# Optimization experiments

Measured on AMD Instinct MI355X. Metric: run time of the kernel, lower is better.

## Reference

```python
import jax, jax.numpy as jnp
import numpy as np

PI = float(np.pi)


def _mat(rows):
    # rows: 4 lists of 4 [..., ] arrays -> [..., 4, 4]
    return jnp.stack([jnp.stack(r, axis=-1) for r in rows], axis=-2)


def _local_frames(q):
    """q: [..., 7] joint angles -> list of 8 local [..., 4, 4] transforms."""
    z = jnp.zeros_like(q[..., 0])
    o = jnp.ones_like(z)

    def cs(a):
        return jnp.cos(a), jnp.sin(a)

    c0, s0 = cs(q[..., 0])
    c1, s1 = cs(q[..., 1])
    c2, s2 = cs(q[..., 2] - 0.5 * PI)
    c3, s3 = cs(q[..., 3])
    c4, s4 = cs(q[..., 4])
    c5, s5 = cs(q[..., 5] + 0.5 * PI)
    c6, s6 = cs(q[..., 6] - 0.5 * PI)

    m0 = _mat([[c0, -s0, z, z], [s0, c0, z, z], [z, z, o, z], [z, z, z, o]])
    m1 = _mat([[c1, -s1, z, z], [z, z, -o, z], [s1, c1, z, z], [z, z, z, o]])
    m2 = _mat([[c2, -s2, z, z], [z, z, o, 0.4 * o], [-s2, -c2, z, z], [z, z, z, o]])
    m3 = _mat([[c3, -s3, z, z], [z, z, -o, z], [s3, c3, z, z], [z, z, z, o]])
    m4 = _mat([[-c4, s4, z, z], [z, z, o, 0.39 * o], [s4, c4, z, z], [z, z, z, o]])
    m5 = _mat([[c5, -s5, z, z], [z, z, -o, z], [s5, c5, z, z], [z, z, z, o]])
    m6 = _mat([[c6, -s6, z, z], [z, z, -o, z], [s6, c6, z, z], [z, z, z, o]])
    m7 = _mat([[-o, z, z, z], [z, z, o, 0.118 * o], [z, o, z, z], [z, z, z, o]])
    return [m0, m1, m2, m3, m4, m5, m6, m7]


def setup_inputs() -> dict:
    key = jax.random.key(0)
    x = jax.random.normal(key, (2000000, 7), dtype=jnp.float32)
    return {"x": x}


def reference(x):
    mats = _local_frames(x)
    frames = [mats[0]]
    f = mats[0]
    for m in mats[1:]:  # fixed chain of 7 tiny 4x4 matmuls over batch
        f = jnp.einsum("...ij,...jk->...ik", f, m)
        frames.append(f)
    return jnp.stack(frames, axis=-3)  # [..., 8, 4, 4]
```

## Files before the change

kernel.cpp:

```cpp
#include <hip/hip_runtime.h>

namespace {

struct V3 { float x, y, z; };

__device__ inline V3 v3(float x, float y, float z) { return {x, y, z}; }
__device__ inline V3 vadd(V3 a, V3 b) { return {a.x + b.x, a.y + b.y, a.z + b.z}; }
__device__ inline V3 vsub(V3 a, V3 b) { return {a.x - b.x, a.y - b.y, a.z - b.z}; }
__device__ inline V3 vmul(float s, V3 a) { return {s * a.x, s * a.y, s * a.z}; }
__device__ inline V3 vneg(V3 a) { return {-a.x, -a.y, -a.z}; }

__device__ inline void stage_frame(float4* p, V3 c0, V3 c1, V3 c2, V3 c3) {
    p[0] = make_float4(c0.x, c1.x, c2.x, c3.x);
    p[1] = make_float4(c0.y, c1.y, c2.y, c3.y);
    p[2] = make_float4(c0.z, c1.z, c2.z, c3.z);
    p[3] = make_float4(0.f, 0.f, 0.f, 1.f);
}

}

#define LPAD 9

__global__ __launch_bounds__(256) void fk_chain_kernel(const float* __restrict__ q,
                                                       float4* __restrict__ out,
                                                       int n)
{
    __shared__ float4 lds[4 * 64 * LPAD];

    const int tid  = threadIdx.x;
    const int lane = tid & 63;
    const int wave = tid >> 6;
    const long long e0 = (long long)blockIdx.x * 256 + (long long)wave * 64;
    if (e0 >= n) return;
    const long long i = e0 + lane;
    const bool active = i < (long long)n;

    const float* qi = q + (active ? i : 0) * 7;
    const float HPI = 1.57079632679489662f;

    float qv[7];
    #pragma unroll
    for (int k = 0; k < 7; ++k) qv[k] = qi[k];

    float c[7], s[7];
    __sincosf(qv[0], &s[0], &c[0]);
    __sincosf(qv[1], &s[1], &c[1]);
    __sincosf(qv[2] - HPI, &s[2], &c[2]);
    __sincosf(qv[3], &s[3], &c[3]);
    __sincosf(qv[4], &s[4], &c[4]);
    __sincosf(qv[5] + HPI, &s[5], &c[5]);
    __sincosf(qv[6] - HPI, &s[6], &c[6]);

    float4* ldsW = lds + wave * (64 * LPAD);
    float4* myS  = ldsW + lane * LPAD;

    const int rk = lane & 7;
    const int re = lane >> 3;
    float4* gb = out + e0 * 32 + (long long)re * 32 + rk;

    V3 f0 = v3(c[0], s[0], 0.f);
    V3 f1 = v3(-s[0], c[0], 0.f);
    V3 f2 = v3(0.f, 0.f, 1.f);
    V3 f3 = v3(0.f, 0.f, 0.f);

    #define TYPE_A(cc, ss)                                 \
        {                                                  \
            V3 t0 = vadd(vmul((cc), f0), vmul((ss), f2));  \
            V3 t1 = vsub(vmul((cc), f2), vmul((ss), f0));  \
            V3 t2 = vneg(f1);                              \
            f0 = t0; f1 = t1; f2 = t2;                     \
        }

    #define FLUSH(p)                                                      \
        {                                                                 \
            _Pragma("unroll")                                             \
            for (int j = 0; j < 8; ++j) {                                 \
                int e = j * 8 + re;                                       \
                float4 v = ldsW[e * LPAD + rk];                           \
                if (e0 + e < (long long)n) gb[(long long)j * 256 + (p) * 8] = v; \
            }                                                             \
        }

    stage_frame(myS + 0, f0, f1, f2, f3);
    TYPE_A(c[1], s[1]);
    stage_frame(myS + 4, f0, f1, f2, f3);
    FLUSH(0);

    {
        V3 t0 = vsub(vmul(c[2], f0), vmul(s[2], f2));
        V3 t1 = vneg(vadd(vmul(s[2], f0), vmul(c[2], f2)));
        V3 t2 = f1;
        f3 = vadd(vmul(0.4f, f1), f3);
        f0 = t0; f1 = t1; f2 = t2;
    }
    stage_frame(myS + 0, f0, f1, f2, f3);
    TYPE_A(c[3], s[3]);
    stage_frame(myS + 4, f0, f1, f2, f3);
    FLUSH(1);

    {
        V3 t0 = vsub(vmul(s[4], f2), vmul(c[4], f0));
        V3 t1 = vadd(vmul(s[4], f0), vmul(c[4], f2));
        V3 t2 = f1;
        f3 = vadd(vmul(0.39f, f1), f3);
        f0 = t0; f1 = t1; f2 = t2;
    }
    stage_frame(myS + 0, f0, f1, f2, f3);
    TYPE_A(c[5], s[5]);
    stage_frame(myS + 4, f0, f1, f2, f3);
    FLUSH(2);

    TYPE_A(c[6], s[6]);
    stage_frame(myS + 0, f0, f1, f2, f3);
    {
        V3 t0 = vneg(f0);
        V3 t1 = f2;
        V3 t2 = f1;
        f3 = vadd(vmul(0.118f, f1), f3);
        f0 = t0; f1 = t1; f2 = t2;
    }
    stage_frame(myS + 4, f0, f1, f2, f3);
    FLUSH(3);

    #undef TYPE_A
    #undef FLUSH
}

extern "C" void kernel_launch(void* const* d_in, const int* in_sizes, int n_in,
                              void* d_out, int out_size, void* d_ws, size_t ws_size,
                              hipStream_t stream) {
    const float* x = (const float*)d_in[0];
    float* out = (float*)d_out;
    int n = in_sizes[0] / 7;
    int block = 256;
    int grid = (n + block - 1) / block;
    fk_chain_kernel<<<grid, block, 0, stream>>>(x, (float4*)out, n);
}
```

Before: 211.6 us.

## Stage all eight frames in LDS then write one coalesced contiguous block

Each element's 8 frames are staged in LDS at a padded stride. After one barrier the 64-thread block writes its 32 KB output region contiguously, replacing the four interleaved partial flushes. Blocks shrink to a single wave and out-of-range lanes read a valid input row. The write is already bandwidth-bound, so the cleaner write pattern may help only a little, while the larger per-block LDS and the barrier could reduce overlap.

```diff
diff --git a/kernel.cpp b/kernel.cpp
--- a/kernel.cpp
+++ b/kernel.cpp
@@ -19,23 +19,20 @@
 
 }
 
-#define LPAD 9
+#define LSTRIDE 33
 
-__global__ __launch_bounds__(256) void fk_chain_kernel(const float* __restrict__ q,
-                                                       float4* __restrict__ out,
-                                                       int n)
+__global__ __launch_bounds__(64) void fk_chain_kernel(const float* __restrict__ q,
+                                                      float4* __restrict__ out,
+                                                      int n)
 {
-    __shared__ float4 lds[4 * 64 * LPAD];
+    __shared__ float4 lds[64 * LSTRIDE];
 
-    const int tid  = threadIdx.x;
-    const int lane = tid & 63;
-    const int wave = tid >> 6;
-    const long long e0 = (long long)blockIdx.x * 256 + (long long)wave * 64;
-    if (e0 >= n) return;
+    const int lane = threadIdx.x;
+    const long long e0 = (long long)blockIdx.x * 64;
     const long long i = e0 + lane;
     const bool active = i < (long long)n;
 
-    const float* qi = q + (active ? i : 0) * 7;
+    const float* qi = q + (active ? i : (long long)(n - 1)) * 7;
     const float HPI = 1.57079632679489662f;
 
     float qv[7];
@@ -51,12 +48,7 @@
     __sincosf(qv[5] + HPI, &s[5], &c[5]);
     __sincosf(qv[6] - HPI, &s[6], &c[6]);
 
-    float4* ldsW = lds + wave * (64 * LPAD);
-    float4* myS  = ldsW + lane * LPAD;
-
-    const int rk = lane & 7;
-    const int re = lane >> 3;
-    float4* gb = out + e0 * 32 + (long long)re * 32 + rk;
+    float4* myS = lds + lane * LSTRIDE;
 
     V3 f0 = v3(c[0], s[0], 0.f);
     V3 f1 = v3(-s[0], c[0], 0.f);
@@ -71,20 +63,10 @@
             f0 = t0; f1 = t1; f2 = t2;                     \
         }
 
-    #define FLUSH(p)                                                      \
-        {                                                                 \
-            _Pragma("unroll")                                             \
-            for (int j = 0; j < 8; ++j) {                                 \
-                int e = j * 8 + re;                                       \
-                float4 v = ldsW[e * LPAD + rk];                           \
-                if (e0 + e < (long long)n) gb[(long long)j * 256 + (p) * 8] = v; \
-            }                                                             \
-        }
+    stage_frame(myS + 0, f0, f1, f2, f3);
 
-    stage_frame(myS + 0, f0, f1, f2, f3);
     TYPE_A(c[1], s[1]);
     stage_frame(myS + 4, f0, f1, f2, f3);
-    FLUSH(0);
 
     {
         V3 t0 = vsub(vmul(c[2], f0), vmul(s[2], f2));
@@ -93,10 +75,10 @@
         f3 = vadd(vmul(0.4f, f1), f3);
         f0 = t0; f1 = t1; f2 = t2;
     }
-    stage_frame(myS + 0, f0, f1, f2, f3);
+    stage_frame(myS + 8, f0, f1, f2, f3);
+
     TYPE_A(c[3], s[3]);
-    stage_frame(myS + 4, f0, f1, f2, f3);
-    FLUSH(1);
+    stage_frame(myS + 12, f0, f1, f2, f3);
 
     {
         V3 t0 = vsub(vmul(s[4], f2), vmul(c[4], f0));
@@ -105,13 +87,14 @@
         f3 = vadd(vmul(0.39f, f1), f3);
         f0 = t0; f1 = t1; f2 = t2;
     }
-    stage_frame(myS + 0, f0, f1, f2, f3);
+    stage_frame(myS + 16, f0, f1, f2, f3);
+
     TYPE_A(c[5], s[5]);
-    stage_frame(myS + 4, f0, f1, f2, f3);
-    FLUSH(2);
+    stage_frame(myS + 20, f0, f1, f2, f3);
 
     TYPE_A(c[6], s[6]);
-    stage_frame(myS + 0, f0, f1, f2, f3);
+    stage_frame(myS + 24, f0, f1, f2, f3);
+
     {
         V3 t0 = vneg(f0);
         V3 t1 = f2;
@@ -119,11 +102,27 @@
         f3 = vadd(vmul(0.118f, f1), f3);
         f0 = t0; f1 = t1; f2 = t2;
     }
-    stage_frame(myS + 4, f0, f1, f2, f3);
-    FLUSH(3);
+    stage_frame(myS + 28, f0, f1, f2, f3);
 
     #undef TYPE_A
-    #undef FLUSH
+
+    __syncthreads();
+
+    float4* gb = out + e0 * 32;
+    if (e0 + 64 <= (long long)n) {
+        #pragma unroll
+        for (int j = 0; j < 32; ++j) {
+            int flat = j * 64 + lane;
+            gb[flat] = lds[(flat >> 5) * LSTRIDE + (flat & 31)];
+        }
+    } else {
+        #pragma unroll
+        for (int j = 0; j < 32; ++j) {
+            int flat = j * 64 + lane;
+            if (e0 + (flat >> 5) < (long long)n)
+                gb[flat] = lds[(flat >> 5) * LSTRIDE + (flat & 31)];
+        }
+    }
 }
 
 extern "C" void kernel_launch(void* const* d_in, const int* in_sizes, int n_in,
@@ -132,7 +131,6 @@
     const float* x = (const float*)d_in[0];
     float* out = (float*)d_out;
     int n = in_sizes[0] / 7;
-    int block = 256;
-    int grid = (n + block - 1) / block;
-    fk_chain_kernel<<<grid, block, 0, stream>>>(x, (float4*)out, n);
+    int grid = (n + 63) / 64;
+    fk_chain_kernel<<<grid, 64, 0, stream>>>(x, (float4*)out, n);
 }
```

Result: faster. 192.8 us (-8.9%).
